# Kernel optimization log

Measured on AMD Instinct MI355X. Metric: run time of the kernel, lower is better.

The kernel has to match this reference:

```python
import jax, jax.numpy as jnp
import numpy as np

DIM, NHEADS, HEAD_DIM = 1536, 12, 128
EPS = 1e-6
ROPE_SPLIT = (22, 21, 21)  # head_dim//2 = 64 -> (c-2*(c//3), c//3, c//3)


def setup_inputs() -> dict:
    key = jax.random.key(0)
    ks = jax.random.split(key, 12)
    B, F, H, W = 1, 8, 16, 28
    L = F * H * W  # 3584
    inp = {
        "x": jax.random.normal(ks[0], (B, L, DIM), jnp.float32),
        "seq_lens": jnp.full((B,), L, dtype=jnp.int64),
        "grid_sizes": jnp.array([[F, H, W]] * B, dtype=jnp.int64),
        "freqs": jax.random.uniform(ks[1], (1024, HEAD_DIM // 2), jnp.float32) * (2 * np.pi),
        "Wq": jax.random.normal(ks[2], (DIM, DIM), jnp.float32) / np.sqrt(DIM),
        "bq": jnp.zeros((DIM,), jnp.float32),
        "Wk": jax.random.normal(ks[3], (DIM, DIM), jnp.float32) / np.sqrt(DIM),
        "bk": jnp.zeros((DIM,), jnp.float32),
        "Wv": jax.random.normal(ks[4], (DIM, DIM), jnp.float32) / np.sqrt(DIM),
        "bv": jnp.zeros((DIM,), jnp.float32),
        "Wo": jax.random.normal(ks[5], (DIM, DIM), jnp.float32) / np.sqrt(DIM),
        "bo": jnp.zeros((DIM,), jnp.float32),
        "gq": jnp.ones((DIM,), jnp.float32),
        "gk": jnp.ones((DIM,), jnp.float32),
    }
    return inp


def _rms_norm(x, g):
    var = jnp.mean(jnp.square(x), axis=-1, keepdims=True)
    return x * jax.lax.rsqrt(var + EPS) * g


def _rope_angles(freqs, F, H, W):
    # freqs: [1024, 64] angles; split per 3D axis and broadcast over the grid
    cf, ch, cw = ROPE_SPLIT
    af = freqs[:F, :cf]
    ah = freqs[:H, cf:cf + ch]
    aw = freqs[:W, cf + ch:]
    ang = jnp.concatenate([
        jnp.broadcast_to(af[:, None, None, :], (F, H, W, cf)),
        jnp.broadcast_to(ah[None, :, None, :], (F, H, W, ch)),
        jnp.broadcast_to(aw[None, None, :, :], (F, H, W, cw)),
    ], axis=-1).reshape(F * H * W, cf + ch + cw)  # [L, 64]
    return jnp.cos(ang), jnp.sin(ang)


def _rope_apply(x, cos, sin):
    # x: [B, L, N, D]; complex multiply by unit-modulus freqs, in real arithmetic
    b, s, n, d = x.shape
    xr = x.reshape(b, s, n, d // 2, 2)
    a, bi = xr[..., 0], xr[..., 1]
    c = cos[None, :, None, :]
    si = sin[None, :, None, :]
    out = jnp.stack([a * c - bi * si, a * si + bi * c], axis=-1)
    return out.reshape(b, s, n, d)


def reference(x, seq_lens, grid_sizes, freqs, Wq, bq, Wk, bk, Wv, bv, Wo, bo, gq, gk):
    b, s, _ = x.shape
    n, d = NHEADS, HEAD_DIM
    gs = np.asarray(grid_sizes)
    F, H, W = int(gs[0, 0]), int(gs[0, 1]), int(gs[0, 2])  # static grid (same per batch)

    q = _rms_norm(x @ Wq + bq, gq).reshape(b, s, n, d)
    k = _rms_norm(x @ Wk + bk, gk).reshape(b, s, n, d)
    v = (x @ Wv + bv).reshape(b, s, n, d)

    cos, sin = _rope_angles(freqs, F, H, W)
    q = _rope_apply(q, cos, sin)
    k = _rope_apply(k, cos, sin)

    # full attention with key-length masking (flash_attention k_lens semantics)
    scale = 1.0 / np.sqrt(d)
    scores = jnp.einsum("bqnd,bknd->bnqk", q, k) * scale
    key_mask = jnp.arange(s)[None, :] < seq_lens[:, None]  # [B, S]
    scores = jnp.where(key_mask[:, None, None, :], scores, -1e9)
    probs = jax.nn.softmax(scores, axis=-1)
    out = jnp.einsum("bnqk,bknd->bqnd", probs, v)

    return out.reshape(b, s, n * d) @ Wo + bo
```

## Files before the change

kernel.cpp:

```cpp
#include <hip/hip_runtime.h>

typedef __bf16 bf16;
typedef __bf16 bf16x8 __attribute__((ext_vector_type(8)));
typedef __bf16 bf16x4 __attribute__((ext_vector_type(4)));
typedef float f32x4 __attribute__((ext_vector_type(4)));

__device__ __forceinline__ void gload_lds16(const void* g, void* l) {
  __builtin_amdgcn_global_load_lds(
      (const __attribute__((address_space(1))) void*)g,
      (__attribute__((address_space(3))) void*)l, 16, 0, 0);
}

__device__ __forceinline__ bf16x8 ld8(const bf16* p) {
  bf16x8 v; __builtin_memcpy(&v, p, 16); return v;
}

__global__ __launch_bounds__(256) void cast_f32_bf16(const float* __restrict__ in,
                                                     bf16* __restrict__ out, int n8) {
  int i = blockIdx.x * 256 + threadIdx.x;
  if (i >= n8) return;
  const float4* p = (const float4*)in + (size_t)i * 2;
  float4 a = p[0], b = p[1];
  bf16x8 o;
  o[0] = (bf16)a.x; o[1] = (bf16)a.y; o[2] = (bf16)a.z; o[3] = (bf16)a.w;
  o[4] = (bf16)b.x; o[5] = (bf16)b.y; o[6] = (bf16)b.z; o[7] = (bf16)b.w;
  *((bf16x8*)out + i) = o;
}

__global__ __launch_bounds__(256) void transpose_w(const float* __restrict__ W,
                                                   bf16* __restrict__ Wt) {
  __shared__ bf16 tile[64][72];
  int t = threadIdx.x;
  int k0 = blockIdx.x * 64, n0 = blockIdx.y * 64;
  int r = t >> 2, c0 = (t & 3) * 16;
  const float* src = W + (size_t)(k0 + r) * 1536 + n0 + c0;
#pragma unroll
  for (int q = 0; q < 4; ++q) {
    float4 v = *(const float4*)(src + q * 4);
    tile[c0 + q * 4 + 0][r] = (bf16)v.x;
    tile[c0 + q * 4 + 1][r] = (bf16)v.y;
    tile[c0 + q * 4 + 2][r] = (bf16)v.z;
    tile[c0 + q * 4 + 3][r] = (bf16)v.w;
  }
  __syncthreads();
  bf16* dst = Wt + (size_t)(n0 + r) * 1536 + k0 + c0;
  bf16x8 o0, o1;
#pragma unroll
  for (int j = 0; j < 8; ++j) { o0[j] = tile[r][c0 + j]; o1[j] = tile[r][c0 + 8 + j]; }
  *(bf16x8*)dst = o0;
  *(bf16x8*)(dst + 8) = o1;
}

__global__ void concat_bias(const float* __restrict__ bq, const float* __restrict__ bk,
                            const float* __restrict__ bv, float* __restrict__ o) {
  int t = blockIdx.x * 256 + threadIdx.x;
  if (t < 1536) o[t] = bq[t];
  else if (t < 3072) o[t] = bk[t - 1536];
  else if (t < 4608) o[t] = bv[t - 3072];
}

template <typename OUT>
__global__ __launch_bounds__(256, 2) void gemm_bt(const bf16* __restrict__ A, const bf16* __restrict__ B,
                                                  const float* __restrict__ bias, OUT* __restrict__ C,
                                                  int M, int N, int K) {
  __shared__ bf16 As[128 * 32], Bs[128 * 32];
  int t = threadIdx.x, l = t & 63, w = t >> 6;
  int lane15 = l & 15, lhi = l >> 4;
  int m0 = blockIdx.x * 128, n0 = blockIdx.y * 128;
  int wm = (w >> 1) * 64, wn = (w & 1) * 64;
  f32x4 zero = {0.f, 0.f, 0.f, 0.f};
  f32x4 acc[4][4];
#pragma unroll
  for (int i = 0; i < 4; ++i)
#pragma unroll
    for (int j = 0; j < 4; ++j) acc[i][j] = zero;

  int srow = t >> 2, scol = (t & 3) * 8;
  const bf16* gA0 = A + (size_t)(m0 + srow) * K + scol;
  const bf16* gA1 = A + (size_t)(m0 + 64 + srow) * K + scol;
  const bf16* gB0 = B + (size_t)(n0 + srow) * K + scol;
  const bf16* gB1 = B + (size_t)(n0 + 64 + srow) * K + scol;
  char* ldsA = (char*)As + (size_t)w * 1024;
  char* ldsB = (char*)Bs + (size_t)w * 1024;

  for (int kt = 0; kt < K; kt += 32) {
    gload_lds16(gA0 + kt, ldsA);
    gload_lds16(gA1 + kt, ldsA + 4096);
    gload_lds16(gB0 + kt, ldsB);
    gload_lds16(gB1 + kt, ldsB + 4096);
    __syncthreads();
    bf16x8 af[4], bfr[4];
#pragma unroll
    for (int i = 0; i < 4; ++i) {
      af[i]  = ld8(&As[(wm + i * 16 + lane15) * 32 + lhi * 8]);
      bfr[i] = ld8(&Bs[(wn + i * 16 + lane15) * 32 + lhi * 8]);
    }
#pragma unroll
    for (int i = 0; i < 4; ++i)
#pragma unroll
      for (int j = 0; j < 4; ++j)
        acc[i][j] = __builtin_amdgcn_mfma_f32_16x16x32_bf16(af[i], bfr[j], acc[i][j], 0, 0, 0);
    __syncthreads();
  }
#pragma unroll
  for (int i = 0; i < 4; ++i)
#pragma unroll
    for (int j = 0; j < 4; ++j) {
      int col = n0 + wn + j * 16 + lane15;
      float bb = bias[col];
#pragma unroll
      for (int r = 0; r < 4; ++r) {
        int row = m0 + wm + i * 16 + lhi * 4 + r;
        C[(size_t)row * N + col] = (OUT)(acc[i][j][r] + bb);
      }
    }
}

__global__ void rope_tab(const float* __restrict__ freqs, const int* __restrict__ gs,
                         float* __restrict__ tabc, float* __restrict__ tabs) {
  int idx = blockIdx.x * 256 + threadIdx.x;
  if (idx >= 3584 * 64) return;
  int s = idx >> 6, i = idx & 63;
  int H = gs[1], W = gs[2];
  int f = s / (H * W);
  int rem = s - f * (H * W);
  int hh = rem / W;
  int ww = rem - hh * W;
  int row = (i < 22) ? f : ((i < 43) ? hh : ww);
  float a = freqs[row * 64 + i];
  tabc[idx] = cosf(a);
  tabs[idx] = sinf(a);
}

__global__ __launch_bounds__(256) void postproc(const bf16* __restrict__ QKV,
    const float* __restrict__ gq, const float* __restrict__ gk,
    const float* __restrict__ tabc, const float* __restrict__ tabs,
    bf16* __restrict__ qb, bf16* __restrict__ kb) {
  int s = blockIdx.x, t = threadIdx.x;
  const bf16* Qr = QKV + (size_t)s * 4608;
  const bf16* Kr = Qr + 1536;
  int j0 = t * 6;
  float qv[6], kv[6];
  float sq = 0.f, sk = 0.f;
#pragma unroll
  for (int j = 0; j < 6; ++j) {
    float a = (float)Qr[j0 + j]; qv[j] = a; sq += a * a;
    float b = (float)Kr[j0 + j]; kv[j] = b; sk += b * b;
  }
#pragma unroll
  for (int off = 32; off > 0; off >>= 1) {
    sq += __shfl_down(sq, off);
    sk += __shfl_down(sk, off);
  }
  __shared__ float red[2][4];
  if ((t & 63) == 0) { red[0][t >> 6] = sq; red[1][t >> 6] = sk; }
  __syncthreads();
  float vq = (red[0][0] + red[0][1]) + (red[0][2] + red[0][3]);
  float vk = (red[1][0] + red[1][1]) + (red[1][2] + red[1][3]);
  float rq = 1.0f / sqrtf(vq * (1.0f / 1536.0f) + 1e-6f);
  float rk = 1.0f / sqrtf(vk * (1.0f / 1536.0f) + 1e-6f);
#pragma unroll
  for (int j = 0; j < 6; j += 2) {
    int jj = j0 + j;
    int d = jj & 127, i = d >> 1, h = jj >> 7;
    float c = tabc[s * 64 + i], sn = tabs[s * 64 + i];
    size_t base = (((size_t)h * 3584 + s) << 7) + d;
    float a = qv[j] * rq * gq[jj], b = qv[j + 1] * rq * gq[jj + 1];
    qb[base] = (bf16)(a * c - b * sn);
    qb[base + 1] = (bf16)(a * sn + b * c);
    float ak = kv[j] * rk * gk[jj], bk2 = kv[j + 1] * rk * gk[jj + 1];
    kb[base] = (bf16)(ak * c - bk2 * sn);
    kb[base + 1] = (bf16)(ak * sn + bk2 * c);
  }
}

__global__ __launch_bounds__(256) void transpose_v(const bf16* __restrict__ QKV,
                                                   bf16* __restrict__ vT) {
  __shared__ bf16 tile[128][72];
  int t = threadIdx.x;
  int h = blockIdx.y;
  int s0 = blockIdx.x * 64;
  int r = t >> 2, c0 = (t & 3) * 32;
  const bf16* src = QKV + (size_t)(s0 + r) * 4608 + 3072 + h * 128 + c0;
#pragma unroll
  for (int q = 0; q < 4; ++q) {
    bf16x8 v = ld8(src + q * 8);
#pragma unroll
    for (int j = 0; j < 8; ++j) tile[c0 + q * 8 + j][r] = v[j];
  }
  __syncthreads();
  int d = t >> 1, sp = (t & 1) * 32;
  bf16* dst = vT + (size_t)(h * 128 + d) * 3584 + s0 + sp;
#pragma unroll
  for (int q = 0; q < 4; ++q) {
    bf16x8 o;
#pragma unroll
    for (int j = 0; j < 8; ++j) o[j] = tile[d][sp + q * 8 + j];
    *(bf16x8*)(dst + q * 8) = o;
  }
}

__global__ __launch_bounds__(256, 2) void flash_attn(
    const bf16* __restrict__ qb, const bf16* __restrict__ kb, const bf16* __restrict__ vT,
    const int* __restrict__ sl, float* __restrict__ po0, float* __restrict__ po1,
    float* __restrict__ ml) {
  const int L = 3584;
  __shared__ bf16 Ks[2][64 * 128];
  __shared__ bf16 Vs[2][128 * 64];
  int t = threadIdx.x, l = t & 63, w = t >> 6;
  int lane15 = l & 15, lhi = l >> 4;
  int grp48 = l & 48;
  int h = blockIdx.y, z = blockIdx.z;
  int qw = blockIdx.x * 128 + w * 32;
  int seqlen = sl[0];
  const float scale = 0.08838834764831845f;
  float* po = z ? po1 : po0;
  float* mlz = ml + (size_t)z * 12 * L * 2;

  bf16x8 aq[2][4];
#pragma unroll
  for (int qf = 0; qf < 2; ++qf)
#pragma unroll
    for (int kc = 0; kc < 4; ++kc)
      aq[qf][kc] = ld8(qb + (((size_t)h * L + qw + qf * 16 + lane15) << 7) + kc * 32 + lhi * 8);

  f32x4 zero = {0.f, 0.f, 0.f, 0.f};
  f32x4 out[2][8];
  float m2[2] = {-1e30f, -1e30f}, ls2[2] = {0.f, 0.f};
#pragma unroll
  for (int qf = 0; qf < 2; ++qf)
#pragma unroll
    for (int df = 0; df < 8; ++df) out[qf][df] = zero;

  int nt = (seqlen + 63) >> 6;
  if (nt > 56) nt = 56;
  int t0 = z * 28, t1 = t0 + 28;
  if (t1 > nt) t1 = nt;

  int rk_s = t >> 4, ck_s = (t & 15) * 16;
  int rv_s = t >> 3;
  int mm = t & 7;
  int sA = 32 * (mm >> 2) + 16 * (mm & 1) + 4 * ((mm >> 1) & 1);
  int oA = 2 * sA;
  int swzk = (rk_s & 7) << 4;
  int swzv = (rv_s & 7) << 4;

  bf16x8 kreg[4], vreg[4];
  if (t0 < t1) {
    int kv0 = t0 * 64;
#pragma unroll
    for (int p = 0; p < 4; ++p) {
      kreg[p] = ld8(kb + (((size_t)h * L + kv0 + p * 16 + rk_s) << 7) + (ck_s >> 1));
      vreg[p] = ld8(vT + (size_t)(h * 128 + p * 32 + rv_s) * L + kv0 + mm * 8);
    }
  }

  int buf = 0;
  for (int ti = t0; ti < t1; ++ti) {
    int kv0 = ti * 64;
#pragma unroll
    for (int p = 0; p < 4; ++p) {
      __builtin_memcpy((char*)Ks[buf] + (p * 16 + rk_s) * 256 + (ck_s ^ swzk), &kreg[p], 16);
      bf16x4 lo, hi;
#pragma unroll
      for (int j = 0; j < 4; ++j) { lo[j] = vreg[p][j]; hi[j] = vreg[p][j + 4]; }
      char* vrow = (char*)Vs[buf] + (p * 32 + rv_s) * 128;
      __builtin_memcpy(vrow + (oA ^ swzv), &lo, 8);
      __builtin_memcpy(vrow + ((oA + 16) ^ swzv), &hi, 8);
    }
    if (ti + 1 < t1) {
      int kn = (ti + 1) * 64;
#pragma unroll
      for (int p = 0; p < 4; ++p) {
        kreg[p] = ld8(kb + (((size_t)h * L + kn + p * 16 + rk_s) << 7) + (ck_s >> 1));
        vreg[p] = ld8(vT + (size_t)(h * 128 + p * 32 + rv_s) * L + kn + mm * 8);
      }
    }
    __syncthreads();

    f32x4 sc[2][4];
#pragma unroll
    for (int qf = 0; qf < 2; ++qf)
#pragma unroll
      for (int a = 0; a < 4; ++a) sc[qf][a] = zero;
#pragma unroll
    for (int a = 0; a < 4; ++a) {
      int rk = a * 16 + lane15;
      const char* krow = (const char*)Ks[buf] + rk * 256;
      int swz = (rk & 7) << 4;
#pragma unroll
      for (int kc = 0; kc < 4; ++kc) {
        bf16x8 bk_ = ld8((const bf16*)(krow + ((kc * 64 + lhi * 16) ^ swz)));
        sc[0][a] = __builtin_amdgcn_mfma_f32_16x16x32_bf16(bk_, aq[0][kc], sc[0][a], 0, 0, 0);
        sc[1][a] = __builtin_amdgcn_mfma_f32_16x16x32_bf16(bk_, aq[1][kc], sc[1][a], 0, 0, 0);
      }
    }

    bool full = (kv0 + 64 <= seqlen);
    bf16x8 ap[2][2];
#pragma unroll
    for (int qf = 0; qf < 2; ++qf) {
      float tm = -1e30f;
#pragma unroll
      for (int a = 0; a < 4; ++a)
#pragma unroll
        for (int r = 0; r < 4; ++r) {
          float s = sc[qf][a][r] * scale;
          if (!full) {
            int col = kv0 + a * 16 + lhi * 4 + r;
            s = (col < seqlen) ? s : -1e30f;
          }
          sc[qf][a][r] = s;
          tm = fmaxf(tm, s);
        }
      tm = fmaxf(tm, __shfl_xor(tm, 16));
      tm = fmaxf(tm, __shfl_xor(tm, 32));
      if (!__all(tm <= m2[qf] + 8.0f)) {
        float nm = fmaxf(m2[qf], tm);
        float f = __expf(m2[qf] - nm);
        m2[qf] = nm;
        ls2[qf] *= f;
#pragma unroll
        for (int r = 0; r < 4; ++r) {
          float fr = __shfl(f, grp48 | (lhi * 4 + r));
#pragma unroll
          for (int df = 0; df < 8; ++df) out[qf][df][r] *= fr;
        }
      }
      float psum = 0.f;
#pragma unroll
      for (int a = 0; a < 4; ++a)
#pragma unroll
        for (int r = 0; r < 4; ++r) {
          float p = __expf(sc[qf][a][r] - m2[qf]);
          sc[qf][a][r] = p;
          psum += p;
        }
      psum += __shfl_xor(psum, 16);
      psum += __shfl_xor(psum, 32);
      ls2[qf] += psum;
#pragma unroll
      for (int c = 0; c < 2; ++c) {
        bf16x8 f8;
#pragma unroll
        for (int r = 0; r < 4; ++r) {
          f8[r] = (bf16)sc[qf][2 * c][r];
          f8[r + 4] = (bf16)sc[qf][2 * c + 1][r];
        }
        ap[qf][c] = f8;
      }
    }

#pragma unroll
    for (int df = 0; df < 8; ++df) {
      int rd = df * 16 + lane15;
      const char* vrow2 = (const char*)Vs[buf] + rd * 128;
      int swz = (rd & 7) << 4;
#pragma unroll
      for (int c = 0; c < 2; ++c) {
        bf16x8 bv_ = ld8((const bf16*)(vrow2 + ((c * 64 + lhi * 16) ^ swz)));
        out[0][df] = __builtin_amdgcn_mfma_f32_16x16x32_bf16(ap[0][c], bv_, out[0][df], 0, 0, 0);
        out[1][df] = __builtin_amdgcn_mfma_f32_16x16x32_bf16(ap[1][c], bv_, out[1][df], 0, 0, 0);
      }
    }
    buf ^= 1;
  }

#pragma unroll
  for (int qf = 0; qf < 2; ++qf) {
#pragma unroll
    for (int r = 0; r < 4; ++r) {
      int row = qw + qf * 16 + lhi * 4 + r;
      size_t rbase = ((size_t)h * L + row) << 7;
#pragma unroll
      for (int df = 0; df < 8; ++df)
        po[rbase + df * 16 + lane15] = out[qf][df][r];
    }
    if (lhi == 0) {
      int row = qw + qf * 16 + lane15;
      mlz[(((size_t)h * L + row) << 1)] = m2[qf];
      mlz[(((size_t)h * L + row) << 1) + 1] = ls2[qf];
    }
  }
}

__global__ __launch_bounds__(256) void combine_halves(
    const float* __restrict__ po0, const float* __restrict__ po1,
    const float* __restrict__ ml, bf16* __restrict__ attn) {
  const int L = 3584;
  int row = blockIdx.x * 8 + (threadIdx.x >> 5);
  int c0 = (threadIdx.x & 31) * 4;
  const float* ml0 = ml;
  const float* ml1 = ml + (size_t)12 * L * 2;
  float m0 = ml0[row * 2], l0 = ml0[row * 2 + 1];
  float m1 = ml1[row * 2], l1 = ml1[row * 2 + 1];
  float M = fmaxf(m0, m1);
  float w0 = __expf(m0 - M), w1 = __expf(m1 - M);
  float inv = 1.0f / fmaxf(w0 * l0 + w1 * l1, 1e-30f);
  float4 a = *(const float4*)(po0 + (size_t)row * 128 + c0);
  float4 b = *(const float4*)(po1 + (size_t)row * 128 + c0);
  int h = row / L, s = row % L;
  bf16x4 o;
  o[0] = (bf16)((w0 * a.x + w1 * b.x) * inv);
  o[1] = (bf16)((w0 * a.y + w1 * b.y) * inv);
  o[2] = (bf16)((w0 * a.z + w1 * b.z) * inv);
  o[3] = (bf16)((w0 * a.w + w1 * b.w) * inv);
  *(bf16x4*)(attn + (size_t)s * 1536 + h * 128 + c0) = o;
}

extern "C" void kernel_launch(void* const* d_in, const int* in_sizes, int n_in,
                              void* d_out, int out_size, void* d_ws, size_t ws_size,
                              hipStream_t stream) {
  const float* x = (const float*)d_in[0];
  const int* seq_lens = (const int*)d_in[1];
  const int* grid_sizes = (const int*)d_in[2];
  const float* freqs = (const float*)d_in[3];
  const float* Wq = (const float*)d_in[4];
  const float* bq = (const float*)d_in[5];
  const float* Wk = (const float*)d_in[6];
  const float* bk = (const float*)d_in[7];
  const float* Wv = (const float*)d_in[8];
  const float* bv = (const float*)d_in[9];
  const float* Wo = (const float*)d_in[10];
  const float* bo = (const float*)d_in[11];
  const float* gq = (const float*)d_in[12];
  const float* gk = (const float*)d_in[13];

  char* ws = (char*)d_ws;
  bf16* x_bf = (bf16*)(ws + 0);
  bf16* wqkvt = (bf16*)(ws + 11010048);
  bf16* wot = (bf16*)(ws + 25165824);
  float* bqkv = (float*)(ws + 29884416);
  bf16* QKV = (bf16*)(ws + 29902848);
  bf16* qb = (bf16*)(ws + 62932992);
  bf16* kb = (bf16*)(ws + 73943040);
  bf16* vT = (bf16*)(ws + 84953088);
  float* tabc = (float*)(ws + 95963136);
  float* tabs = (float*)(ws + 96880640);
  float* po0 = (float*)(ws + 29902848);
  bf16* attn = (bf16*)(ws + 51922944);
  float* po1 = (float*)(ws + 0);
  float* ml  = (float*)(ws + 95963136);

  cast_f32_bf16<<<2688, 256, 0, stream>>>(x, x_bf, 688128);
  transpose_w<<<dim3(24, 24), 256, 0, stream>>>(Wq, wqkvt);
  transpose_w<<<dim3(24, 24), 256, 0, stream>>>(Wk, wqkvt + 1536 * 1536);
  transpose_w<<<dim3(24, 24), 256, 0, stream>>>(Wv, wqkvt + 2 * 1536 * 1536);
  transpose_w<<<dim3(24, 24), 256, 0, stream>>>(Wo, wot);
  concat_bias<<<18, 256, 0, stream>>>(bq, bk, bv, bqkv);
  rope_tab<<<896, 256, 0, stream>>>(freqs, grid_sizes, tabc, tabs);
  gemm_bt<bf16><<<dim3(28, 36), 256, 0, stream>>>(x_bf, wqkvt, bqkv, QKV, 3584, 4608, 1536);
  postproc<<<3584, 256, 0, stream>>>(QKV, gq, gk, tabc, tabs, qb, kb);
  transpose_v<<<dim3(56, 12), 256, 0, stream>>>(QKV, vT);
  flash_attn<<<dim3(28, 12, 2), 256, 0, stream>>>(qb, kb, vT, seq_lens, po0, po1, ml);
  combine_halves<<<5376, 256, 0, stream>>>(po0, po1, ml, attn);
  gemm_bt<float><<<dim3(28, 12), 256, 0, stream>>>(attn, wot, bo, (float*)d_out, 3584, 1536, 1536);
}
```

Before: 276.6 us.

## Single-buffer flash-attn LDS, use exp2 softmax, and raise priority around MFMA loops

Shrinks the K/V shared-memory staging from double to single buffer, adding a barrier before each tile's LDS write so the previous tile's reads finish first. This halves LDS per block, which can allow more resident blocks. The softmax folds log2(e) into the scale and uses exp2f with an adjusted lazy-rescale threshold, and the combine kernel uses exp2f to match. s_setprio is raised around the MFMA sections so waves doing matrix work get scheduling priority. The trade-off is an extra barrier per iteration and less overlap between LDS writes and compute.

New measurement: 299.9 us. 1.08x slower.

```diff
diff --git a/kernel.cpp b/kernel.cpp
--- a/kernel.cpp
+++ b/kernel.cpp
@@ -205,15 +205,16 @@
     const int* __restrict__ sl, float* __restrict__ po0, float* __restrict__ po1,
     float* __restrict__ ml) {
   const int L = 3584;
-  __shared__ bf16 Ks[2][64 * 128];
-  __shared__ bf16 Vs[2][128 * 64];
-  int t = threadIdx.x, l = t & 63, w = t >> 6;
+  __shared__ bf16 Ks[64 * 128];
+  __shared__ bf16 Vs[128 * 64];
+  int t = threadIdx.x, l = t & 63;
   int lane15 = l & 15, lhi = l >> 4;
   int grp48 = l & 48;
   int h = blockIdx.y, z = blockIdx.z;
+  int w = t >> 6;
   int qw = blockIdx.x * 128 + w * 32;
   int seqlen = sl[0];
-  const float scale = 0.08838834764831845f;
+  const float scale = 0.08838834764831845f * 1.44269504088896340f;
   float* po = z ? po1 : po0;
   float* mlz = ml + (size_t)z * 12 * L * 2;
 
@@ -255,19 +256,20 @@
     }
   }
 
-  int buf = 0;
   for (int ti = t0; ti < t1; ++ti) {
     int kv0 = ti * 64;
+    __syncthreads();
 #pragma unroll
     for (int p = 0; p < 4; ++p) {
-      __builtin_memcpy((char*)Ks[buf] + (p * 16 + rk_s) * 256 + (ck_s ^ swzk), &kreg[p], 16);
+      __builtin_memcpy((char*)Ks + (p * 16 + rk_s) * 256 + (ck_s ^ swzk), &kreg[p], 16);
       bf16x4 lo, hi;
 #pragma unroll
       for (int j = 0; j < 4; ++j) { lo[j] = vreg[p][j]; hi[j] = vreg[p][j + 4]; }
-      char* vrow = (char*)Vs[buf] + (p * 32 + rv_s) * 128;
+      char* vrow = (char*)Vs + (p * 32 + rv_s) * 128;
       __builtin_memcpy(vrow + (oA ^ swzv), &lo, 8);
       __builtin_memcpy(vrow + ((oA + 16) ^ swzv), &hi, 8);
     }
+    __syncthreads();
     if (ti + 1 < t1) {
       int kn = (ti + 1) * 64;
 #pragma unroll
@@ -276,17 +278,17 @@
         vreg[p] = ld8(vT + (size_t)(h * 128 + p * 32 + rv_s) * L + kn + mm * 8);
       }
     }
-    __syncthreads();
 
     f32x4 sc[2][4];
 #pragma unroll
     for (int qf = 0; qf < 2; ++qf)
 #pragma unroll
       for (int a = 0; a < 4; ++a) sc[qf][a] = zero;
+    __builtin_amdgcn_s_setprio(1);
 #pragma unroll
     for (int a = 0; a < 4; ++a) {
       int rk = a * 16 + lane15;
-      const char* krow = (const char*)Ks[buf] + rk * 256;
+      const char* krow = (const char*)Ks + rk * 256;
       int swz = (rk & 7) << 4;
 #pragma unroll
       for (int kc = 0; kc < 4; ++kc) {
@@ -295,6 +297,7 @@
         sc[1][a] = __builtin_amdgcn_mfma_f32_16x16x32_bf16(bk_, aq[1][kc], sc[1][a], 0, 0, 0);
       }
     }
+    __builtin_amdgcn_s_setprio(0);
 
     bool full = (kv0 + 64 <= seqlen);
     bf16x8 ap[2][2];
@@ -315,9 +318,9 @@
         }
       tm = fmaxf(tm, __shfl_xor(tm, 16));
       tm = fmaxf(tm, __shfl_xor(tm, 32));
-      if (!__all(tm <= m2[qf] + 8.0f)) {
+      if (!__all(tm <= m2[qf] + 11.54f)) {
         float nm = fmaxf(m2[qf], tm);
-        float f = __expf(m2[qf] - nm);
+        float f = exp2f(m2[qf] - nm);
         m2[qf] = nm;
         ls2[qf] *= f;
 #pragma unroll
@@ -332,7 +335,7 @@
       for (int a = 0; a < 4; ++a)
 #pragma unroll
         for (int r = 0; r < 4; ++r) {
-          float p = __expf(sc[qf][a][r] - m2[qf]);
+          float p = exp2f(sc[qf][a][r] - m2[qf]);
           sc[qf][a][r] = p;
           psum += p;
         }
@@ -351,10 +354,11 @@
       }
     }
 
+    __builtin_amdgcn_s_setprio(1);
 #pragma unroll
     for (int df = 0; df < 8; ++df) {
       int rd = df * 16 + lane15;
-      const char* vrow2 = (const char*)Vs[buf] + rd * 128;
+      const char* vrow2 = (const char*)Vs + rd * 128;
       int swz = (rd & 7) << 4;
 #pragma unroll
       for (int c = 0; c < 2; ++c) {
@@ -363,7 +367,7 @@
         out[1][df] = __builtin_amdgcn_mfma_f32_16x16x32_bf16(ap[1][c], bv_, out[1][df], 0, 0, 0);
       }
     }
-    buf ^= 1;
+    __builtin_amdgcn_s_setprio(0);
   }
 
 #pragma unroll
@@ -395,7 +399,7 @@
   float m0 = ml0[row * 2], l0 = ml0[row * 2 + 1];
   float m1 = ml1[row * 2], l1 = ml1[row * 2 + 1];
   float M = fmaxf(m0, m1);
-  float w0 = __expf(m0 - M), w1 = __expf(m1 - M);
+  float w0 = exp2f(m0 - M), w1 = exp2f(m1 - M);
   float inv = 1.0f / fmaxf(w0 * l0 + w1 * l1, 1e-30f);
   float4 a = *(const float4*)(po0 + (size_t)row * 128 + c0);
   float4 b = *(const float4*)(po1 + (size_t)row * 128 + c0);
```
